# Performance work log

Measured on AMD Instinct MI355X. Metric: run time of the kernel, lower is better.

## Reference

```python
import jax, jax.numpy as jnp
import numpy as np

B, H, W = 8, 256, 256
NF = 64          # num_feat
E = 12           # num_expert
D = NF * 4       # token dim = 256
CD = D * E       # expanded dim = 3072


def _lrelu(x):
    return jnp.where(x >= 0, x, 0.2 * x)


def _conv(x, w, stride, pad):
    return jax.lax.conv_general_dilated(
        x, w, (stride, stride), [(pad, pad), (pad, pad)],
        dimension_numbers=('NCHW', 'OIHW', 'NCHW'))


def _bn(x, g, b):
    # training-mode BatchNorm2d: batch statistics over (N, H, W)
    m = jnp.mean(x, axis=(0, 2, 3), keepdims=True)
    v = jnp.var(x, axis=(0, 2, 3), keepdims=True)
    xn = (x - m) * jax.lax.rsqrt(v + 1e-5)
    return xn * g[None, :, None, None] + b[None, :, None, None]


def setup_inputs() -> dict:
    key = jax.random.key(0)
    ks = jax.random.split(key, 16)
    s = 0.05
    d = {}
    d['x'] = jax.random.normal(ks[0], (B, 3, H, W), jnp.float32)
    d['conv0_w'] = jax.random.normal(ks[1], (NF, 3, 3, 3)) * s
    d['conv0_b'] = jnp.zeros((NF,))
    d['conv1_w'] = jax.random.normal(ks[2], (NF, NF, 4, 4)) * s
    d['bn1_g'] = jnp.ones((NF,)); d['bn1_b'] = jnp.zeros((NF,))
    d['conv2_w'] = jax.random.normal(ks[3], (2 * NF, NF, 3, 3)) * s
    d['bn2_g'] = jnp.ones((2 * NF,)); d['bn2_b'] = jnp.zeros((2 * NF,))
    d['conv3_w'] = jax.random.normal(ks[4], (2 * NF, 2 * NF, 4, 4)) * s
    d['bn3_g'] = jnp.ones((2 * NF,)); d['bn3_b'] = jnp.zeros((2 * NF,))
    d['conv4_w'] = jax.random.normal(ks[5], (4 * NF, 2 * NF, 3, 3)) * s
    d['bn4_g'] = jnp.ones((4 * NF,)); d['bn4_b'] = jnp.zeros((4 * NF,))
    d['conv5_w'] = jax.random.normal(ks[6], (4 * NF, 4 * NF, 3, 3)) * s
    d['bn5_g'] = jnp.ones((4 * NF,)); d['bn5_b'] = jnp.zeros((4 * NF,))
    d['conv6_w'] = jax.random.normal(ks[7], (4 * NF, 4 * NF, 3, 3)) * s
    d['bn6_g'] = jnp.ones((4 * NF,)); d['bn6_b'] = jnp.zeros((4 * NF,))
    d['w_gating'] = jax.random.normal(ks[8], (D, E))          # torch.randn init
    d['body_w'] = jax.random.normal(ks[9], (D, CD)) * s       # Linear(c_dim, c_dim*blocks)
    d['body_b'] = jnp.zeros((CD,))
    d['ortho_w'] = jax.random.normal(ks[10], (1, 1, CD))      # OrthorTransform weight
    d['cls_w1'] = jax.random.normal(ks[11], (D, NF // 2)) * s # shared classifier
    d['cls_b1'] = jnp.zeros((NF // 2,))
    d['cls_w2'] = jax.random.normal(ks[12], (NF // 2, 1)) * s
    d['cls_b2'] = jnp.zeros((1,))
    return d


def reference(x, conv0_w, conv0_b, conv1_w, bn1_g, bn1_b, conv2_w, bn2_g, bn2_b,
              conv3_w, bn3_g, bn3_b, conv4_w, bn4_g, bn4_b, conv5_w, bn5_g, bn5_b,
              conv6_w, bn6_g, bn6_b, w_gating, body_w, body_b, ortho_w,
              cls_w1, cls_b1, cls_w2, cls_b2):
    # --- FE conv stack ---
    h = _lrelu(_conv(x, conv0_w, 1, 1) + conv0_b[None, :, None, None])
    h = _lrelu(_bn(_conv(h, conv1_w, 2, 1), bn1_g, bn1_b))
    h = _lrelu(_bn(_conv(h, conv2_w, 1, 1), bn2_g, bn2_b))
    h = _lrelu(_bn(_conv(h, conv3_w, 2, 1), bn3_g, bn3_b))
    h = _lrelu(_bn(_conv(h, conv4_w, 1, 1), bn4_g, bn4_b))
    h = _lrelu(_bn(_conv(h, conv5_w, 1, 1), bn5_g, bn5_b))
    h = _lrelu(_bn(_conv(h, conv6_w, 1, 1), bn6_g, bn6_b))
    b, c, hh, ww = h.shape
    tok = h.reshape(b, c, hh * ww).transpose(0, 2, 1)            # (B, N, D)
    # --- softmax router ---
    routing = jax.nn.softmax(jnp.einsum('bnd,de->bne', tok, w_gating), axis=-1)
    # --- CodeReduction: Linear + lrelu, OrthorTransform multiply, lrelu ---
    feat = _lrelu(tok @ body_w + body_b)                         # (B, N, E*D)
    feat = _lrelu(feat * ortho_w)
    feat = feat.reshape(b, hh * ww, E, D)                        # torch.split chunks
    # --- shared expert MLP on every chunk (all classifiers alias one module) ---
    hid = _lrelu(jnp.einsum('bned,df->bnef', feat, cls_w1) + cls_b1)
    outs = (jnp.einsum('bnef,fo->bneo', hid, cls_w2) + cls_b2)[..., 0]  # (B,N,E)
    # --- top-1 select (equivalent to the torch.where cascade) ---
    idx = jnp.argmax(routing, axis=-1, keepdims=True)
    output = jnp.take_along_axis(outs, idx, axis=-1)             # (B, N, 1)
    return output
```

## Files before the change

### kernel.cpp

```cpp
#include <hip/hip_runtime.h>

__device__ __forceinline__ float lrelu(float x) { return x >= 0.f ? x : 0.2f * x; }

typedef const __attribute__((address_space(1))) void* gas_ptr;
typedef __attribute__((address_space(3))) void* las_ptr;

__global__ __launch_bounds__(256) void conv0_k(const float* __restrict__ x,
                                               const float* __restrict__ w,
                                               const float* __restrict__ bias,
                                               float* __restrict__ out) {
    __shared__ float sIn[3][34][34];
    __shared__ float sW[27][16];
    const int H = 256;
    int tid = threadIdx.x, tx = tid & 31, ty = tid >> 5;
    int tX = (blockIdx.x & 7) * 32, tY = (blockIdx.x >> 3) * 32;
    int b = blockIdx.y, cog = blockIdx.z * 16;
    float acc[4][16] = {};
    const float* inB = x + (size_t)b * 3 * H * H;
    for (int idx = tid; idx < 3 * 1156; idx += 256) {
        int ci = idx / 1156, r = idx % 1156, iy = r / 34, ix = r % 34;
        int gy = tY - 1 + iy, gx = tX - 1 + ix;
        float v = 0.f;
        if ((unsigned)gy < 256u && (unsigned)gx < 256u)
            v = inB[(ci * H + gy) * H + gx];
// ... 3 lines not shown
        int co = idx & 15, rest = idx >> 4;
        sW[rest][co] = w[(cog + co) * 27 + rest];
    }
    __syncthreads();
#pragma unroll
    for (int ci = 0; ci < 3; ci++)
#pragma unroll
        for (int dy = 0; dy < 3; dy++)
#pragma unroll
            for (int dx = 0; dx < 3; dx++) {
                float a0 = sIn[ci][ty + dy][tx + dx];
                float a1 = sIn[ci][ty + 8 + dy][tx + dx];
                float a2 = sIn[ci][ty + 16 + dy][tx + dx];
                float a3 = sIn[ci][ty + 24 + dy][tx + dx];
                const float* wp = sW[ci * 9 + dy * 3 + dx];
#pragma unroll
                for (int co = 0; co < 16; co++) {
                    float wv = wp[co];
                    acc[0][co] += a0 * wv; acc[1][co] += a1 * wv;
                    acc[2][co] += a2 * wv; acc[3][co] += a3 * wv;
                }
            }
    float* outB = out + (size_t)(b * 64 + cog) * 67080;
#pragma unroll
    for (int co = 0; co < 16; co++) {
        float bv = bias[cog + co];
#pragma unroll
        for (int r = 0; r < 4; r++)
            outB[(size_t)co * 67080 + (size_t)(tY + ty + 8 * r + 1) * 260 +
                 tX + tx + 1] = lrelu(acc[r][co] + bv);
    }
}

template <int COG>
__device__ __forceinline__ void stats_epilogue(float (&acc)[4][COG], float* red,
                                               double2* part, int cog,
                                               int slotBase, int S, int tid) {
#pragma unroll
    for (int c = 0; c < COG; c++) {
        float s = 0.f, q = 0.f;
#pragma unroll
        for (int j = 0; j < 4; j++) { float v = acc[j][c]; s += v; q += v * v; }
        red[c * 256 + tid] = s;
        red[COG * 256 + c * 256 + tid] = q;
    }
    __syncthreads();
    for (int off = 128; off; off >>= 1) {
        if (tid < off) {
#pragma unroll
            for (int c = 0; c < COG; c++) {
                red[c * 256 + tid] += red[c * 256 + tid + off];
                red[COG * 256 + c * 256 + tid] +=
                    red[COG * 256 + c * 256 + tid + off];
            }
        }
        __syncthreads();
    }
    if (tid < COG) {
        int slot = slotBase + blockIdx.y * gridDim.x + blockIdx.x;
        part[(size_t)(cog + tid) * S + slot].x = (double)red[tid * 256];
        part[(size_t)(cog + tid) * S + slot].y =
            (double)red[COG * 256 + tid * 256];
    }
}

template <int COG>
__global__ __launch_bounds__(256) void c4x4p_k(const float* __restrict__ in,
                                               const float* __restrict__ w,
                                               float* __restrict__ out,
                                               double2* __restrict__ part,
                                               int slotBase, int S,
                                               int Cin, int Cout, int Hin,
                                               int Hp, int Wp,
                                               int oHp, int oWp, int oOff) {
    __shared__ float sIn[2][4488];
    __shared__ float sW[2][16 * COG];
    const int Hout = Hin >> 1;
    const int tid = threadIdx.x, tx = tid & 31, ty = tid >> 5;
    const int tpr = Hout >> 5;
    const int tX = (blockIdx.x % tpr) * 32, tY = (blockIdx.x / tpr) * 32;
    const int b = blockIdx.y, cog = blockIdx.z * COG;
    const int HWin = Hp * Wp;
    const float* inB = in + (size_t)b * Cin * HWin;
    const int wvbase = tid & ~63;

    int gOff[5]; int lOff[5]; bool act[5];
#pragma unroll
    for (int r = 0; r < 5; r++) {
        int idx = tid + r * 256;
        bool a = idx < 1122;
        int row = idx / 17, c4 = idx % 17;
        gOff[r] = a ? ((2 * tY + row) * Wp + 2 * tX + 4 * c4) : 0;
        lOff[r] = (r * 256 + wvbase) * 4;
        act[r] = a;
    }
    const int wco = tid % COG, wt = tid / COG;
    const int wgo = ((cog + wco) * Cin) * 16 + wt;
    const bool wact = tid < 16 * COG;

    float acc[4][COG];
#pragma unroll
    for (int j = 0; j < 4; j++)
#pragma unroll
        for (int c = 0; c < COG; c++) acc[j][c] = 0.f;

#pragma unroll
    for (int r = 0; r < 5; r++)
        if (act[r])
            __builtin_amdgcn_global_load_lds((gas_ptr)(inB + gOff[r]),
                                             (las_ptr)(&sIn[0][lOff[r]]), 16, 0, 0);
    if (wact)
        __builtin_amdgcn_global_load_lds((gas_ptr)(w + wgo),
                                         (las_ptr)(&sW[0][wvbase]), 4, 0, 0);
    __syncthreads();

    for (int k = 0; k < Cin; k++) {
        const int cur = k & 1, nb = cur ^ 1;
        const bool more = (k + 1) < Cin;
        if (more) {
            const float* p = inB + (size_t)(k + 1) * HWin;
#pragma unroll
            for (int r = 0; r < 5; r++)
                if (act[r])
                    __builtin_amdgcn_global_load_lds(
                        (gas_ptr)(p + gOff[r]),
                        (las_ptr)(&sIn[nb][lOff[r]]), 16, 0, 0);
            if (wact)
                __builtin_amdgcn_global_load_lds(
                    (gas_ptr)(w + wgo + (k + 1) * 16),
                    (las_ptr)(&sW[nb][wvbase]), 4, 0, 0);
        }
        const float* sI = sIn[cur];
        const float* sw = sW[cur];
#pragma unroll
        for (int dy = 0; dy < 4; dy++)
#pragma unroll
            for (int dx = 0; dx < 4; dx++) {
                const float* bp = sI + (2 * ty + dy) * 68 + 2 * tx + dx;
                float a0 = bp[0];
                float a1 = bp[16 * 68];
                float a2 = bp[32 * 68];
                float a3 = bp[48 * 68];
                const float* wp = sw + (dy * 4 + dx) * COG;
#pragma unroll
                for (int c = 0; c < COG; c++) {
                    float wv = wp[c];
                    acc[0][c] += a0 * wv; acc[1][c] += a1 * wv;
                    acc[2][c] += a2 * wv; acc[3][c] += a3 * wv;
                }
            }
        __syncthreads();
    }

    float* outB = out + (size_t)(b * Cout + cog) * oHp * oWp;
#pragma unroll
    for (int c = 0; c < COG; c++)
#pragma unroll
        for (int r = 0; r < 4; r++)
            outB[(size_t)c * oHp * oWp +
                 (size_t)(tY + ty + 8 * r + oOff) * oWp + tX + tx + oOff] =
                acc[r][c];
    stats_epilogue<COG>(acc, &sIn[0][0], part, cog, slotBase, S, tid);
}

template <int COG>
__global__ __launch_bounds__(256) void c3x3_k(const float* __restrict__ in,
                                              const float* __restrict__ w,
                                              float* __restrict__ out,
                                              double2* __restrict__ part,
                                              int slotBase, int S,
                                              int Cin, int Cout, int H,
                                              int Hp, int Wp,
                                              int oHp, int oWp, int oOff) {
    constexpr int RS = 36;
    constexpr int CI = 34 * RS;
    __shared__ float sIn[2][2 * CI];
    __shared__ float sW[2][18 * COG];
    const int tid = threadIdx.x, tx = tid & 31, ty = tid >> 5;
    const int tpr = H >> 5;
    const int tX = (blockIdx.x % tpr) * 32, tY = (blockIdx.x / tpr) * 32;
    const int b = blockIdx.y, cog = blockIdx.z * COG;
    const int HWin = Hp * Wp;
    const float* inB = in + (size_t)b * Cin * HWin;
    const int wvbase = tid & ~63;

    int gOff[3]; int lOff[3]; bool act[3];
#pragma unroll
    for (int r = 0; r < 3; r++) {
        int idx = tid + r * 256;
        bool a = idx < 612;
        int ci = idx / 306, rem = idx % 306;
        int row = rem / 9, c4 = rem % 9;
        gOff[r] = a ? (ci * HWin + (tY + row) * Wp + tX + 4 * c4) : 0;
        lOff[r] = (r * 256 + wvbase) * 4;
        act[r] = a;
    }
    constexpr int NW = (18 * COG + 255) / 256;
    int wgo[NW]; bool wact[NW];
#pragma unroll
    for (int r = 0; r < NW; r++) {
        int widx = tid + r * 256;
        bool a = widx < 18 * COG;
        int co = widx % COG, rest = widx / COG;
        int ci = rest / 9, t = rest % 9;
        wgo[r] = a ? (((cog + co) * Cin + ci) * 9 + t) : 0;
        wact[r] = a;
    }

    float acc[4][COG];
#pragma unroll
    for (int j = 0; j < 4; j++)
#pragma unroll
        for (int c = 0; c < COG; c++) acc[j][c] = 0.f;

    const int steps = Cin >> 1;

#pragma unroll
    for (int r = 0; r < 3; r++)
        if (act[r])
            __builtin_amdgcn_global_load_lds(
                (gas_ptr)(inB + gOff[r]),
                (las_ptr)(&sIn[0][lOff[r]]), 16, 0, 0);
#pragma unroll
    for (int r = 0; r < NW; r++)
        if (wact[r])
            __builtin_amdgcn_global_load_lds(
                (gas_ptr)(w + wgo[r]),
                (las_ptr)(&sW[0][r * 256 + wvbase]), 4, 0, 0);
    __syncthreads();

    for (int k = 0; k < steps; k++) {
        const int cur = k & 1;
        const int nb = cur ^ 1;
        const bool more = (k + 1) < steps;
        if (more) {
            const int c0n = 2 * (k + 1);
            const float* p = inB + (size_t)c0n * HWin;
            const float* wp2 = w + (size_t)c0n * 9;
#pragma unroll
            for (int r = 0; r < 3; r++)
                if (act[r])
                    __builtin_amdgcn_global_load_lds(
                        (gas_ptr)(p + gOff[r]),
                        (las_ptr)(&sIn[nb][lOff[r]]), 16, 0, 0);
#pragma unroll
            for (int r = 0; r < NW; r++)
                if (wact[r])
                    __builtin_amdgcn_global_load_lds(
                        (gas_ptr)(wp2 + wgo[r]),
                        (las_ptr)(&sW[nb][r * 256 + wvbase]), 4, 0, 0);
        }
        const float* sI = sIn[cur];
        const float* sw = sW[cur];
#pragma unroll
        for (int ci = 0; ci < 2; ci++)
#pragma unroll
            for (int dx = 0; dx < 3; dx++) {
                const float* bp = sI + ci * CI + (4 * ty) * RS + tx + dx;
                float a[6];
#pragma unroll
                for (int j = 0; j < 6; j++) a[j] = bp[j * RS];
#pragma unroll
                for (int dy = 0; dy < 3; dy++) {
                    const float* wp = sw + (ci * 9 + dy * 3 + dx) * COG;
#pragma unroll
                    for (int c = 0; c < COG; c++) {
                        float wv = wp[c];
                        acc[0][c] += a[0 + dy] * wv;
                        acc[1][c] += a[1 + dy] * wv;
                        acc[2][c] += a[2 + dy] * wv;
                        acc[3][c] += a[3 + dy] * wv;
                    }
                }
            }
        __syncthreads();
    }

    float* outB = out + (size_t)(b * Cout + cog) * oHp * oWp;
#pragma unroll
    for (int c = 0; c < COG; c++)
#pragma unroll
        for (int j = 0; j < 4; j++)
            outB[(size_t)c * oHp * oWp +
                 (size_t)(tY + 4 * ty + j + oOff) * oWp + tX + tx + oOff] =
                acc[j][c];
    stats_epilogue<COG>(acc, &sIn[0][0], part, cog, slotBase, S, tid);
}

__global__ void bnfin_k(const double2* __restrict__ part, int S, int C, double invN,
                        const float* __restrict__ g, const float* __restrict__ bb,
                        float2* __restrict__ ss) {
    int c = threadIdx.x;
    if (c >= C) return;
    double sum = 0.0, sq = 0.0;
    for (int s = 0; s < S; s++) {
        double2 p = part[(size_t)c * S + s];
        sum += p.x; sq += p.y;
    }
    double m = sum * invN;
    double v = sq * invN - m * m;
    double sc = (double)g[c] / sqrt(v + 1e-5);
    ss[c] = make_float2((float)sc, (float)((double)bb[c] - m * sc));
}

__global__ __launch_bounds__(256) void bnact_k(float* __restrict__ p,
                                               const float2* __restrict__ ss,
                                               int C, int H, int W,
                                               int Hp, int Wp) {
    int pc = blockIdx.x;
    int c = pc & (C - 1);
    float2 t = ss ? ss[c] : make_float2(1.f, 0.f);
    bool xf = (ss != nullptr);
    float* pl = p + (size_t)pc * Hp * Wp;
    int n = Hp * Wp;
    for (int i = threadIdx.x; i < n; i += 256) {
        int y = i / Wp, x = i - y * Wp;
        bool inter = (y >= 1) && (y <= H) && (x >= 1) && (x <= W);
        if (!inter) pl[i] = 0.f;
        else if (xf) { float v = pl[i]; pl[i] = lrelu(t.x * v + t.y); }
// ... 113 lines not shown
    const float* g5  = (const float*)d_in[16];
    const float* be5 = (const float*)d_in[17];
    const float* w6  = (const float*)d_in[18];
    const float* g6  = (const float*)d_in[19];
    const float* be6 = (const float*)d_in[20];
    const float* wg  = (const float*)d_in[21];
    const float* bw  = (const float*)d_in[22];
    const float* bbp = (const float*)d_in[23];
    const float* owp = (const float*)d_in[24];
    const float* cw1 = (const float*)d_in[25];
    const float* cb1 = (const float*)d_in[26];
    const float* cw2 = (const float*)d_in[27];
    const float* cb2 = (const float*)d_in[28];

    char* W = (char*)d_ws;
    float2* ssb = (float2*)W;
    float2* ss1 = ssb;
    float2* ss2 = ssb + 64;
    float2* ss3 = ssb + 192;
    float2* ss4 = ssb + 320;
    float2* ss5 = ssb + 576;
    float2* ss6 = ssb + 832;
    double2* part = (double2*)(W + 16384);

    char* BIG = W + 278528;
    float* h0p = (float*)(BIG);
    float* h1p = (float*)(BIG + 70287360);
    float* h2p = (float*)(BIG);
    float* h3p = (float*)(BIG + 70287360);
    float* h4p = (float*)(BIG);
    float* h5p = (float*)(BIG + 36765696);
    float* h6  = (float*)(BIG);
    float* tok = (float*)(BIG + 36765696);

    bnact_k<<<256, 256, 0, stream>>>(h0p, nullptr, 64, 256, 256, 258, 260);
    for (int half = 0; half < 2; half++) {
        conv0_k<<<dim3(64, 4, 4), 256, 0, stream>>>(
            x + (size_t)half * 4 * 3 * 65536, w0, b0, h0p);
        c4x4p_k<8><<<dim3(16, 4, 8), 256, 0, stream>>>(
            h0p, w1, h1p + (size_t)half * 4 * 64 * 17160, part, half * 64, 128,
            64, 64, 256, 258, 260, 130, 132, 1);
    }
    bnfin_k<<<1, 256, 0, stream>>>(part, 128, 64, 1.0 / 131072.0, g1, be1, ss1);
    bnact_k<<<512, 256, 0, stream>>>(h1p, ss1, 64, 128, 128, 130, 132);
    c3x3_k<8><<<dim3(16, 8, 16), 256, 0, stream>>>(
        h1p, w2, h2p, part, 0, 128, 64, 128, 128, 130, 132, 130, 132, 1);
    bnfin_k<<<1, 256, 0, stream>>>(part, 128, 128, 1.0 / 131072.0, g2, be2, ss2);
    bnact_k<<<1024, 256, 0, stream>>>(h2p, ss2, 128, 128, 128, 130, 132);
    c4x4p_k<8><<<dim3(4, 8, 16), 256, 0, stream>>>(
        h2p, w3, h3p, part, 0, 32, 128, 128, 128, 130, 132, 66, 68, 1);
    bnfin_k<<<1, 256, 0, stream>>>(part, 32, 128, 1.0 / 32768.0, g3, be3, ss3);
    bnact_k<<<1024, 256, 0, stream>>>(h3p, ss3, 128, 64, 64, 66, 68);
    c3x3_k<8><<<dim3(4, 8, 32), 256, 0, stream>>>(
        h3p, w4, h4p, part, 0, 32, 128, 256, 64, 66, 68, 66, 68, 1);
    bnfin_k<<<1, 256, 0, stream>>>(part, 32, 256, 1.0 / 32768.0, g4, be4, ss4);
    bnact_k<<<2048, 256, 0, stream>>>(h4p, ss4, 256, 64, 64, 66, 68);
    c3x3_k<8><<<dim3(4, 8, 32), 256, 0, stream>>>(
        h4p, w5, h5p, part, 0, 32, 256, 256, 64, 66, 68, 66, 68, 1);
    bnfin_k<<<1, 256, 0, stream>>>(part, 32, 256, 1.0 / 32768.0, g5, be5, ss5);
    bnact_k<<<2048, 256, 0, stream>>>(h5p, ss5, 256, 64, 64, 66, 68);
    c3x3_k<8><<<dim3(4, 8, 32), 256, 0, stream>>>(
        h5p, w6, h6, part, 0, 32, 256, 256, 64, 66, 68, 64, 64, 0);
    bnfin_k<<<1, 256, 0, stream>>>(part, 32, 256, 1.0 / 32768.0, g6, be6, ss6);
    transp_k<<<dim3(128, 8, 8), 256, 0, stream>>>(h6, ss6, tok);
    token_k<<<8192, 256, 0, stream>>>(tok, wg, bw, bbp, owp, cw1, cb1, cw2, cb2,
                                      (float*)d_out);
}
```

Measured before the change: 2.628 ms.

## Parametrize conv tile height and use wave-shuffle BN stats reduction

Adds a rows-per-thread template parameter to the 4x4 stride-2 and 3x3 conv kernels and launches the smaller 64x64 layers and conv1/conv3 with half-height tiles, doubling block counts for better CU occupancy on small grids. The BN partial-stat epilogue now reduces with wave shuffles and a tiny shared buffer instead of a 256-wide shared-memory tree with many barriers. Halving tile height increases halo reloads and weight traffic per output, and doubles partial-stat slots for bnfin.

```diff
diff --git a/kernel.cpp b/kernel.cpp
--- a/kernel.cpp
+++ b/kernel.cpp
@@ -59,39 +59,43 @@
     }
 }
 
-template <int COG>
-__device__ __forceinline__ void stats_epilogue(float (&acc)[4][COG], float* red,
-                                               double2* part, int cog,
-                                               int slotBase, int S, int tid) {
+template <int COG, int RPT>
+__device__ __forceinline__ void stats_epi(float (&acc)[RPT][COG], float2* sRed,
+                                          double2* part, int cog, int slotBase,
+                                          int S, int tid) {
+    const int lane = tid & 63, wv = tid >> 6;
+    float s[COG], q[COG];
 #pragma unroll
     for (int c = 0; c < COG; c++) {
-        float s = 0.f, q = 0.f;
-#pragma unroll
-        for (int j = 0; j < 4; j++) { float v = acc[j][c]; s += v; q += v * v; }
-        red[c * 256 + tid] = s;
-        red[COG * 256 + c * 256 + tid] = q;
-    }
+        float ss = 0.f, qq = 0.f;
+#pragma unroll
+        for (int j = 0; j < RPT; j++) { float v = acc[j][c]; ss += v; qq += v * v; }
+        s[c] = ss; q[c] = qq;
+    }
+#pragma unroll
+    for (int off = 32; off; off >>= 1)
+#pragma unroll
+        for (int c = 0; c < COG; c++) {
+            s[c] += __shfl_xor(s[c], off);
+            q[c] += __shfl_xor(q[c], off);
+        }
+    if (lane == 0)
+#pragma unroll
+        for (int c = 0; c < COG; c++) sRed[wv * COG + c] = make_float2(s[c], q[c]);
     __syncthreads();
-    for (int off = 128; off; off >>= 1) {
-        if (tid < off) {
-#pragma unroll
-            for (int c = 0; c < COG; c++) {
-                red[c * 256 + tid] += red[c * 256 + tid + off];
-                red[COG * 256 + c * 256 + tid] +=
-                    red[COG * 256 + c * 256 + tid + off];
-            }
+    if (tid < COG) {
+        double ss = 0.0, qq = 0.0;
+#pragma unroll
+        for (int wvi = 0; wvi < 4; wvi++) {
+            float2 p = sRed[wvi * COG + tid];
+            ss += (double)p.x; qq += (double)p.y;
         }
-        __syncthreads();
-    }
-    if (tid < COG) {
         int slot = slotBase + blockIdx.y * gridDim.x + blockIdx.x;
-        part[(size_t)(cog + tid) * S + slot].x = (double)red[tid * 256];
-        part[(size_t)(cog + tid) * S + slot].y =
-            (double)red[COG * 256 + tid * 256];
-    }
-}
-
-template <int COG>
+        part[(size_t)(cog + tid) * S + slot] = make_double2(ss, qq);
+    }
+}
+
+template <int COG, int RPT>
 __global__ __launch_bounds__(256) void c4x4p_k(const float* __restrict__ in,
                                                const float* __restrict__ w,
                                                float* __restrict__ out,
@@ -100,22 +104,27 @@
                                                int Cin, int Cout, int Hin,
                                                int Hp, int Wp,
                                                int oHp, int oWp, int oOff) {
-    __shared__ float sIn[2][4488];
+    constexpr int THo = 8 * RPT;
+    constexpr int ROWS = 16 * RPT + 2;
+    constexpr int NSF4 = ROWS * 17;
+    constexpr int NR = (NSF4 + 255) / 256;
+    __shared__ float sIn[2][ROWS * 68];
     __shared__ float sW[2][16 * COG];
+    __shared__ float2 sRed[4 * COG];
     const int Hout = Hin >> 1;
     const int tid = threadIdx.x, tx = tid & 31, ty = tid >> 5;
-    const int tpr = Hout >> 5;
-    const int tX = (blockIdx.x % tpr) * 32, tY = (blockIdx.x / tpr) * 32;
+    const int tpw = Hout >> 5;
+    const int tX = (blockIdx.x % tpw) * 32, tY = (blockIdx.x / tpw) * THo;
     const int b = blockIdx.y, cog = blockIdx.z * COG;
     const int HWin = Hp * Wp;
     const float* inB = in + (size_t)b * Cin * HWin;
     const int wvbase = tid & ~63;
 
-    int gOff[5]; int lOff[5]; bool act[5];
-#pragma unroll
-    for (int r = 0; r < 5; r++) {
+    int gOff[NR]; int lOff[NR]; bool act[NR];
+#pragma unroll
+    for (int r = 0; r < NR; r++) {
         int idx = tid + r * 256;
-        bool a = idx < 1122;
+        bool a = idx < NSF4;
         int row = idx / 17, c4 = idx % 17;
         gOff[r] = a ? ((2 * tY + row) * Wp + 2 * tX + 4 * c4) : 0;
         lOff[r] = (r * 256 + wvbase) * 4;
@@ -125,14 +134,14 @@
     const int wgo = ((cog + wco) * Cin) * 16 + wt;
     const bool wact = tid < 16 * COG;
 
-    float acc[4][COG];
-#pragma unroll
-    for (int j = 0; j < 4; j++)
+    float acc[RPT][COG];
+#pragma unroll
+    for (int j = 0; j < RPT; j++)
 #pragma unroll
         for (int c = 0; c < COG; c++) acc[j][c] = 0.f;
 
 #pragma unroll
-    for (int r = 0; r < 5; r++)
+    for (int r = 0; r < NR; r++)
         if (act[r])
             __builtin_amdgcn_global_load_lds((gas_ptr)(inB + gOff[r]),
                                              (las_ptr)(&sIn[0][lOff[r]]), 16, 0, 0);
@@ -147,7 +156,7 @@
         if (more) {
             const float* p = inB + (size_t)(k + 1) * HWin;
 #pragma unroll
-            for (int r = 0; r < 5; r++)
+            for (int r = 0; r < NR; r++)
                 if (act[r])
                     __builtin_amdgcn_global_load_lds(
                         (gas_ptr)(p + gOff[r]),
@@ -164,16 +173,15 @@
 #pragma unroll
             for (int dx = 0; dx < 4; dx++) {
                 const float* bp = sI + (2 * ty + dy) * 68 + 2 * tx + dx;
-                float a0 = bp[0];
-                float a1 = bp[16 * 68];
-                float a2 = bp[32 * 68];
-                float a3 = bp[48 * 68];
+                float a[RPT];
+#pragma unroll
+                for (int j = 0; j < RPT; j++) a[j] = bp[j * 16 * 68];
                 const float* wp = sw + (dy * 4 + dx) * COG;
 #pragma unroll
                 for (int c = 0; c < COG; c++) {
                     float wv = wp[c];
-                    acc[0][c] += a0 * wv; acc[1][c] += a1 * wv;
-                    acc[2][c] += a2 * wv; acc[3][c] += a3 * wv;
+#pragma unroll
+                    for (int j = 0; j < RPT; j++) acc[j][c] += a[j] * wv;
                 }
             }
         __syncthreads();
@@ -183,14 +191,14 @@
 #pragma unroll
     for (int c = 0; c < COG; c++)
 #pragma unroll
-        for (int r = 0; r < 4; r++)
+        for (int j = 0; j < RPT; j++)
             outB[(size_t)c * oHp * oWp +
-                 (size_t)(tY + ty + 8 * r + oOff) * oWp + tX + tx + oOff] =
-                acc[r][c];
-    stats_epilogue<COG>(acc, &sIn[0][0], part, cog, slotBase, S, tid);
-}
-
-template <int COG>
+                 (size_t)(tY + ty + 8 * j + oOff) * oWp + tX + tx + oOff] =
+                acc[j][c];
+    stats_epi<COG, RPT>(acc, sRed, part, cog, slotBase, S, tid);
+}
+
+template <int COG, int RPT>
 __global__ __launch_bounds__(256) void c3x3_k(const float* __restrict__ in,
                                               const float* __restrict__ w,
                                               float* __restrict__ out,
@@ -199,24 +207,29 @@
                                               int Cin, int Cout, int H,
                                               int Hp, int Wp,
                                               int oHp, int oWp, int oOff) {
+    constexpr int TH = 8 * RPT;
     constexpr int RS = 36;
-    constexpr int CI = 34 * RS;
+    constexpr int ROWS = TH + 2;
+    constexpr int CI = ROWS * RS;
+    constexpr int NSF4 = 2 * ROWS * 9;
+    constexpr int NR = (NSF4 + 255) / 256;
     __shared__ float sIn[2][2 * CI];
     __shared__ float sW[2][18 * COG];
+    __shared__ float2 sRed[4 * COG];
     const int tid = threadIdx.x, tx = tid & 31, ty = tid >> 5;
-    const int tpr = H >> 5;
-    const int tX = (blockIdx.x % tpr) * 32, tY = (blockIdx.x / tpr) * 32;
+    const int tpw = H >> 5;
+    const int tX = (blockIdx.x % tpw) * 32, tY = (blockIdx.x / tpw) * TH;
     const int b = blockIdx.y, cog = blockIdx.z * COG;
     const int HWin = Hp * Wp;
     const float* inB = in + (size_t)b * Cin * HWin;
     const int wvbase = tid & ~63;
 
-    int gOff[3]; int lOff[3]; bool act[3];
-#pragma unroll
-    for (int r = 0; r < 3; r++) {
+    int gOff[NR]; int lOff[NR]; bool act[NR];
+#pragma unroll
+    for (int r = 0; r < NR; r++) {
         int idx = tid + r * 256;
-        bool a = idx < 612;
-        int ci = idx / 306, rem = idx % 306;
+        bool a = idx < NSF4;
+        int ci = idx / (9 * ROWS), rem = idx % (9 * ROWS);
         int row = rem / 9, c4 = rem % 9;
         gOff[r] = a ? (ci * HWin + (tY + row) * Wp + tX + 4 * c4) : 0;
         lOff[r] = (r * 256 + wvbase) * 4;
@@ -234,16 +247,16 @@
         wact[r] = a;
     }
 
-    float acc[4][COG];
-#pragma unroll
-    for (int j = 0; j < 4; j++)
+    float acc[RPT][COG];
+#pragma unroll
+    for (int j = 0; j < RPT; j++)
 #pragma unroll
         for (int c = 0; c < COG; c++) acc[j][c] = 0.f;
 
     const int steps = Cin >> 1;
 
 #pragma unroll
-    for (int r = 0; r < 3; r++)
+    for (int r = 0; r < NR; r++)
         if (act[r])
             __builtin_amdgcn_global_load_lds(
                 (gas_ptr)(inB + gOff[r]),
@@ -265,7 +278,7 @@
             const float* p = inB + (size_t)c0n * HWin;
             const float* wp2 = w + (size_t)c0n * 9;
 #pragma unroll
-            for (int r = 0; r < 3; r++)
+            for (int r = 0; r < NR; r++)
                 if (act[r])
                     __builtin_amdgcn_global_load_lds(
                         (gas_ptr)(p + gOff[r]),
@@ -283,20 +296,19 @@
         for (int ci = 0; ci < 2; ci++)
 #pragma unroll
             for (int dx = 0; dx < 3; dx++) {
-                const float* bp = sI + ci * CI + (4 * ty) * RS + tx + dx;
-                float a[6];
-#pragma unroll
-                for (int j = 0; j < 6; j++) a[j] = bp[j * RS];
+                const float* bp = sI + ci * CI + (RPT * ty) * RS + tx + dx;
+                float a[RPT + 2];
+#pragma unroll
+                for (int j = 0; j < RPT + 2; j++) a[j] = bp[j * RS];
 #pragma unroll
                 for (int dy = 0; dy < 3; dy++) {
                     const float* wp = sw + (ci * 9 + dy * 3 + dx) * COG;
 #pragma unroll
                     for (int c = 0; c < COG; c++) {
                         float wv = wp[c];
-                        acc[0][c] += a[0 + dy] * wv;
-                        acc[1][c] += a[1 + dy] * wv;
-                        acc[2][c] += a[2 + dy] * wv;
-                        acc[3][c] += a[3 + dy] * wv;
+#pragma unroll
+                        for (int j = 0; j < RPT; j++)
+                            acc[j][c] += a[j + dy] * wv;
                     }
                 }
             }
@@ -307,11 +319,11 @@
 #pragma unroll
     for (int c = 0; c < COG; c++)
 #pragma unroll
-        for (int j = 0; j < 4; j++)
+        for (int j = 0; j < RPT; j++)
             outB[(size_t)c * oHp * oWp +
-                 (size_t)(tY + 4 * ty + j + oOff) * oWp + tX + tx + oOff] =
+                 (size_t)(tY + RPT * ty + j + oOff) * oWp + tX + tx + oOff] =
                 acc[j][c];
-    stats_epilogue<COG>(acc, &sIn[0][0], part, cog, slotBase, S, tid);
+    stats_epi<COG, RPT>(acc, sRed, part, cog, slotBase, S, tid);
 }
 
 __global__ void bnfin_k(const double2* __restrict__ part, int S, int C, double invN,
@@ -496,31 +508,31 @@
     for (int half = 0; half < 2; half++) {
         conv0_k<<<dim3(64, 4, 4), 256, 0, stream>>>(
             x + (size_t)half * 4 * 3 * 65536, w0, b0, h0p);
-        c4x4p_k<8><<<dim3(16, 4, 8), 256, 0, stream>>>(
-            h0p, w1, h1p + (size_t)half * 4 * 64 * 17160, part, half * 64, 128,
+        c4x4p_k<8, 2><<<dim3(32, 4, 8), 256, 0, stream>>>(
+            h0p, w1, h1p + (size_t)half * 4 * 64 * 17160, part, half * 128, 256,
             64, 64, 256, 258, 260, 130, 132, 1);
     }
-    bnfin_k<<<1, 256, 0, stream>>>(part, 128, 64, 1.0 / 131072.0, g1, be1, ss1);
+    bnfin_k<<<1, 256, 0, stream>>>(part, 256, 64, 1.0 / 131072.0, g1, be1, ss1);
     bnact_k<<<512, 256, 0, stream>>>(h1p, ss1, 64, 128, 128, 130, 132);
-    c3x3_k<8><<<dim3(16, 8, 16), 256, 0, stream>>>(
+    c3x3_k<8, 4><<<dim3(16, 8, 16), 256, 0, stream>>>(
         h1p, w2, h2p, part, 0, 128, 64, 128, 128, 130, 132, 130, 132, 1);
     bnfin_k<<<1, 256, 0, stream>>>(part, 128, 128, 1.0 / 131072.0, g2, be2, ss2);
     bnact_k<<<1024, 256, 0, stream>>>(h2p, ss2, 128, 128, 128, 130, 132);
-    c4x4p_k<8><<<dim3(4, 8, 16), 256, 0, stream>>>(
-        h2p, w3, h3p, part, 0, 32, 128, 128, 128, 130, 132, 66, 68, 1);
-    bnfin_k<<<1, 256, 0, stream>>>(part, 32, 128, 1.0 / 32768.0, g3, be3, ss3);
+    c4x4p_k<8, 2><<<dim3(8, 8, 16), 256, 0, stream>>>(
+        h2p, w3, h3p, part, 0, 64, 128, 128, 128, 130, 132, 66, 68, 1);
+    bnfin_k<<<1, 256, 0, stream>>>(part, 64, 128, 1.0 / 32768.0, g3, be3, ss3);
     bnact_k<<<1024, 256, 0, stream>>>(h3p, ss3, 128, 64, 64, 66, 68);
-    c3x3_k<8><<<dim3(4, 8, 32), 256, 0, stream>>>(
-        h3p, w4, h4p, part, 0, 32, 128, 256, 64, 66, 68, 66, 68, 1);
-    bnfin_k<<<1, 256, 0, stream>>>(part, 32, 256, 1.0 / 32768.0, g4, be4, ss4);
+    c3x3_k<8, 2><<<dim3(8, 8, 32), 256, 0, stream>>>(
+        h3p, w4, h4p, part, 0, 64, 128, 256, 64, 66, 68, 66, 68, 1);
+    bnfin_k<<<1, 256, 0, stream>>>(part, 64, 256, 1.0 / 32768.0, g4, be4, ss4);
     bnact_k<<<2048, 256, 0, stream>>>(h4p, ss4, 256, 64, 64, 66, 68);
-    c3x3_k<8><<<dim3(4, 8, 32), 256, 0, stream>>>(
-        h4p, w5, h5p, part, 0, 32, 256, 256, 64, 66, 68, 66, 68, 1);
-    bnfin_k<<<1, 256, 0, stream>>>(part, 32, 256, 1.0 / 32768.0, g5, be5, ss5);
+    c3x3_k<8, 2><<<dim3(8, 8, 32), 256, 0, stream>>>(
+        h4p, w5, h5p, part, 0, 64, 256, 256, 64, 66, 68, 66, 68, 1);
+    bnfin_k<<<1, 256, 0, stream>>>(part, 64, 256, 1.0 / 32768.0, g5, be5, ss5);
     bnact_k<<<2048, 256, 0, stream>>>(h5p, ss5, 256, 64, 64, 66, 68);
-    c3x3_k<8><<<dim3(4, 8, 32), 256, 0, stream>>>(
-        h5p, w6, h6, part, 0, 32, 256, 256, 64, 66, 68, 64, 64, 0);
-    bnfin_k<<<1, 256, 0, stream>>>(part, 32, 256, 1.0 / 32768.0, g6, be6, ss6);
+    c3x3_k<8, 2><<<dim3(8, 8, 32), 256, 0, stream>>>(
+        h5p, w6, h6, part, 0, 64, 256, 256, 64, 66, 68, 64, 64, 0);
+    bnfin_k<<<1, 256, 0, stream>>>(part, 64, 256, 1.0 / 32768.0, g6, be6, ss6);
     transp_k<<<dim3(128, 8, 8), 256, 0, stream>>>(h6, ss6, tok);
     token_k<<<8192, 256, 0, stream>>>(tok, wg, bw, bbp, owp, cw1, cb1, cw2, cb2,
                                       (float*)d_out);
```

Result: slower. 2.756 ms (+4.9%).

## Triple-buffer conv input staging with explicit vmcnt waits and wave-shuffle BN stats

Applied to the files above, without the earlier changes.

The 4x4 stride-2 and 3x3 conv kernels now use a three-stage LDS ring with async global-to-LDS loads issued two steps ahead. Each step waits on a fixed vmcnt count followed by a single s_barrier, replacing the double buffer with a full __syncthreads per step. To keep the per-wave vmcnt counts uniform, waves that would otherwise issue no load for a slot issue a dummy load into a scratch LDS buffer. The BN statistics epilogue is replaced by wave shuffles plus a small cross-wave reduction, removing a long tree of shared-memory stages and barriers. In exchange the kernels use more LDS per block, which may lower occupancy, and the hand-written vmcnt values are fragile.

```diff
diff --git a/kernel.cpp b/kernel.cpp
--- a/kernel.cpp
+++ b/kernel.cpp
@@ -60,34 +60,38 @@
 }
 
 template <int COG>
-__device__ __forceinline__ void stats_epilogue(float (&acc)[4][COG], float* red,
-                                               double2* part, int cog,
-                                               int slotBase, int S, int tid) {
+__device__ __forceinline__ void stats_epi(float (&acc)[4][COG], float2* sRed,
+                                          double2* part, int cog, int slotBase,
+                                          int S, int tid) {
+    const int lane = tid & 63, wv = tid >> 6;
+    float s[COG], q[COG];
 #pragma unroll
     for (int c = 0; c < COG; c++) {
-        float s = 0.f, q = 0.f;
-#pragma unroll
-        for (int j = 0; j < 4; j++) { float v = acc[j][c]; s += v; q += v * v; }
-        red[c * 256 + tid] = s;
-        red[COG * 256 + c * 256 + tid] = q;
-    }
+        float ss = 0.f, qq = 0.f;
+#pragma unroll
+        for (int j = 0; j < 4; j++) { float v = acc[j][c]; ss += v; qq += v * v; }
+        s[c] = ss; q[c] = qq;
+    }
+#pragma unroll
+    for (int off = 32; off; off >>= 1)
+#pragma unroll
+        for (int c = 0; c < COG; c++) {
+            s[c] += __shfl_xor(s[c], off);
+            q[c] += __shfl_xor(q[c], off);
+        }
+    if (lane == 0)
+#pragma unroll
+        for (int c = 0; c < COG; c++) sRed[wv * COG + c] = make_float2(s[c], q[c]);
     __syncthreads();
-    for (int off = 128; off; off >>= 1) {
-        if (tid < off) {
-#pragma unroll
-            for (int c = 0; c < COG; c++) {
-                red[c * 256 + tid] += red[c * 256 + tid + off];
-                red[COG * 256 + c * 256 + tid] +=
-                    red[COG * 256 + c * 256 + tid + off];
-            }
+    if (tid < COG) {
+        double ss = 0.0, qq = 0.0;
+#pragma unroll
+        for (int wvi = 0; wvi < 4; wvi++) {
+            float2 p = sRed[wvi * COG + tid];
+            ss += (double)p.x; qq += (double)p.y;
         }
-        __syncthreads();
-    }
-    if (tid < COG) {
         int slot = slotBase + blockIdx.y * gridDim.x + blockIdx.x;
-        part[(size_t)(cog + tid) * S + slot].x = (double)red[tid * 256];
-        part[(size_t)(cog + tid) * S + slot].y =
-            (double)red[COG * 256 + tid * 256];
+        part[(size_t)(cog + tid) * S + slot] = make_double2(ss, qq);
     }
 }
 
@@ -100,10 +104,14 @@
                                                int Cin, int Cout, int Hin,
                                                int Hp, int Wp,
                                                int oHp, int oWp, int oOff) {
-    __shared__ float sIn[2][4488];
-    __shared__ float sW[2][16 * COG];
+    constexpr int NSF4 = 1122;
+    __shared__ float sIn[3][4488];
+    __shared__ float sW[3][16 * COG];
+    __shared__ float2 sRed[4 * COG];
+    __shared__ alignas(16) float sDummy[64];
     const int Hout = Hin >> 1;
     const int tid = threadIdx.x, tx = tid & 31, ty = tid >> 5;
+    const bool lane0 = (tid & 63) == 0;
     const int tpr = Hout >> 5;
     const int tX = (blockIdx.x % tpr) * 32, tY = (blockIdx.x / tpr) * 32;
     const int b = blockIdx.y, cog = blockIdx.z * COG;
@@ -111,19 +119,20 @@
     const float* inB = in + (size_t)b * Cin * HWin;
     const int wvbase = tid & ~63;
 
-    int gOff[5]; int lOff[5]; bool act[5];
+    int gOff[5]; int lOff[5]; bool act[5]; bool aw[5];
 #pragma unroll
     for (int r = 0; r < 5; r++) {
         int idx = tid + r * 256;
-        bool a = idx < 1122;
+        act[r] = idx < NSF4;
+        aw[r] = (r * 256 + wvbase) < NSF4;
         int row = idx / 17, c4 = idx % 17;
-        gOff[r] = a ? ((2 * tY + row) * Wp + 2 * tX + 4 * c4) : 0;
+        gOff[r] = act[r] ? ((2 * tY + row) * Wp + 2 * tX + 4 * c4) : 0;
         lOff[r] = (r * 256 + wvbase) * 4;
-        act[r] = a;
     }
     const int wco = tid % COG, wt = tid / COG;
     const int wgo = ((cog + wco) * Cin) * 16 + wt;
     const bool wact = tid < 16 * COG;
+    const bool waw = wvbase < 16 * COG;
 
     float acc[4][COG];
 #pragma unroll
@@ -131,32 +140,36 @@
 #pragma unroll
         for (int c = 0; c < COG; c++) acc[j][c] = 0.f;
 
-#pragma unroll
-    for (int r = 0; r < 5; r++)
-        if (act[r])
-            __builtin_amdgcn_global_load_lds((gas_ptr)(inB + gOff[r]),
-                                             (las_ptr)(&sIn[0][lOff[r]]), 16, 0, 0);
-    if (wact)
-        __builtin_amdgcn_global_load_lds((gas_ptr)(w + wgo),
-                                         (las_ptr)(&sW[0][wvbase]), 4, 0, 0);
-    __syncthreads();
-
-    for (int k = 0; k < Cin; k++) {
-        const int cur = k & 1, nb = cur ^ 1;
-        const bool more = (k + 1) < Cin;
-        if (more) {
-            const float* p = inB + (size_t)(k + 1) * HWin;
-#pragma unroll
-            for (int r = 0; r < 5; r++)
-                if (act[r])
-                    __builtin_amdgcn_global_load_lds(
-                        (gas_ptr)(p + gOff[r]),
-                        (las_ptr)(&sIn[nb][lOff[r]]), 16, 0, 0);
-            if (wact)
-                __builtin_amdgcn_global_load_lds(
-                    (gas_ptr)(w + wgo + (k + 1) * 16),
-                    (las_ptr)(&sW[nb][wvbase]), 4, 0, 0);
+    auto STAGE = [&](int t, int buf) {
+        const float* p = inB + (size_t)t * HWin;
+#pragma unroll
+        for (int r = 0; r < 5; r++) {
+            float* dst = act[r] ? &sIn[buf][lOff[r]] : sDummy;
+            const float* src = act[r] ? (p + gOff[r]) : p;
+            if (act[r] || (!aw[r] && lane0))
+                __builtin_amdgcn_global_load_lds((gas_ptr)src, (las_ptr)dst,
+                                                 16, 0, 0);
         }
+        {
+            const float* wsrc = wact ? (w + wgo + t * 16) : w;
+            float* wdst = wact ? &sW[buf][wvbase] : sDummy;
+            if (wact || (!waw && lane0))
+                __builtin_amdgcn_global_load_lds((gas_ptr)wsrc, (las_ptr)wdst,
+                                                 4, 0, 0);
+        }
+    };
+
+    const int steps = Cin;
+    STAGE(0, 0);
+    STAGE(1, 1);
+    int cur = 0, nx2 = 2;
+    for (int k = 0; k < steps; k++) {
+        if (k < steps - 1) asm volatile("s_waitcnt vmcnt(6)" ::: "memory");
+        else               asm volatile("s_waitcnt vmcnt(0)" ::: "memory");
+        __builtin_amdgcn_sched_barrier(0);
+        __builtin_amdgcn_s_barrier();
+        __builtin_amdgcn_sched_barrier(0);
+        if (k + 2 < steps) STAGE(k + 2, nx2);
         const float* sI = sIn[cur];
         const float* sw = sW[cur];
 #pragma unroll
@@ -176,7 +189,8 @@
                     acc[2][c] += a2 * wv; acc[3][c] += a3 * wv;
                 }
             }
-        __syncthreads();
+        cur = (cur == 2) ? 0 : cur + 1;
+        nx2 = (nx2 == 2) ? 0 : nx2 + 1;
     }
 
     float* outB = out + (size_t)(b * Cout + cog) * oHp * oWp;
@@ -187,7 +201,7 @@
             outB[(size_t)c * oHp * oWp +
                  (size_t)(tY + ty + 8 * r + oOff) * oWp + tX + tx + oOff] =
                 acc[r][c];
-    stats_epilogue<COG>(acc, &sIn[0][0], part, cog, slotBase, S, tid);
+    stats_epi<COG>(acc, sRed, part, cog, slotBase, S, tid);
 }
 
 template <int COG>
@@ -201,9 +215,13 @@
                                               int oHp, int oWp, int oOff) {
     constexpr int RS = 36;
     constexpr int CI = 34 * RS;
-    __shared__ float sIn[2][2 * CI];
-    __shared__ float sW[2][18 * COG];
+    constexpr int NSF4 = 612;
+    __shared__ float sIn[3][2 * CI];
+    __shared__ float sW[3][18 * COG];
+    __shared__ float2 sRed[4 * COG];
+    __shared__ alignas(16) float sDummy[64];
     const int tid = threadIdx.x, tx = tid & 31, ty = tid >> 5;
+    const bool lane0 = (tid & 63) == 0;
     const int tpr = H >> 5;
     const int tX = (blockIdx.x % tpr) * 32, tY = (blockIdx.x / tpr) * 32;
     const int b = blockIdx.y, cog = blockIdx.z * COG;
@@ -211,27 +229,24 @@
     const float* inB = in + (size_t)b * Cin * HWin;
     const int wvbase = tid & ~63;
 
-    int gOff[3]; int lOff[3]; bool act[3];
+    int gOff[3]; int lOff[3]; bool act[3]; bool aw[3];
 #pragma unroll
     for (int r = 0; r < 3; r++) {
         int idx = tid + r * 256;
-        bool a = idx < 612;
+        act[r] = idx < NSF4;
+        aw[r] = (r * 256 + wvbase) < NSF4;
         int ci = idx / 306, rem = idx % 306;
         int row = rem / 9, c4 = rem % 9;
-        gOff[r] = a ? (ci * HWin + (tY + row) * Wp + tX + 4 * c4) : 0;
+        gOff[r] = act[r] ? (ci * HWin + (tY + row) * Wp + tX + 4 * c4) : 0;
         lOff[r] = (r * 256 + wvbase) * 4;
-        act[r] = a;
-    }
-    constexpr int NW = (18 * COG + 255) / 256;
-    int wgo[NW]; bool wact[NW];
-#pragma unroll
-    for (int r = 0; r < NW; r++) {
-        int widx = tid + r * 256;
-        bool a = widx < 18 * COG;
-        int co = widx % COG, rest = widx / COG;
+    }
+    const bool wact = tid < 18 * COG;
+    const bool waw = wvbase < 18 * COG;
+    int wgo;
+    {
+        int co = tid % COG, rest = tid / COG;
         int ci = rest / 9, t = rest % 9;
-        wgo[r] = a ? (((cog + co) * Cin + ci) * 9 + t) : 0;
-        wact[r] = a;
+        wgo = ((cog + co) * Cin + ci) * 9 + t;
     }
 
     float acc[4][COG];
@@ -240,43 +255,36 @@
 #pragma unroll
         for (int c = 0; c < COG; c++) acc[j][c] = 0.f;
 
+    auto STAGE = [&](int t, int buf) {
+        const float* p = inB + (size_t)(2 * t) * HWin;
+#pragma unroll
+        for (int r = 0; r < 3; r++) {
+            float* dst = act[r] ? &sIn[buf][lOff[r]] : sDummy;
+            const float* src = act[r] ? (p + gOff[r]) : p;
+            if (act[r] || (!aw[r] && lane0))
+                __builtin_amdgcn_global_load_lds((gas_ptr)src, (las_ptr)dst,
+                                                 16, 0, 0);
+        }
+        {
+            const float* wsrc = wact ? (w + (size_t)(2 * t) * 9 + wgo) : w;
+            float* wdst = wact ? &sW[buf][wvbase] : sDummy;
+            if (wact || (!waw && lane0))
+                __builtin_amdgcn_global_load_lds((gas_ptr)wsrc, (las_ptr)wdst,
+                                                 4, 0, 0);
+        }
+    };
+
     const int steps = Cin >> 1;
-
-#pragma unroll
-    for (int r = 0; r < 3; r++)
-        if (act[r])
-            __builtin_amdgcn_global_load_lds(
-                (gas_ptr)(inB + gOff[r]),
-                (las_ptr)(&sIn[0][lOff[r]]), 16, 0, 0);
-#pragma unroll
-    for (int r = 0; r < NW; r++)
-        if (wact[r])
-            __builtin_amdgcn_global_load_lds(
-                (gas_ptr)(w + wgo[r]),
-                (las_ptr)(&sW[0][r * 256 + wvbase]), 4, 0, 0);
-    __syncthreads();
-
+    STAGE(0, 0);
+    STAGE(1, 1);
+    int cur = 0, nx2 = 2;
     for (int k = 0; k < steps; k++) {
-        const int cur = k & 1;
-        const int nb = cur ^ 1;
-        const bool more = (k + 1) < steps;
-        if (more) {
-            const int c0n = 2 * (k + 1);
-            const float* p = inB + (size_t)c0n * HWin;
-            const float* wp2 = w + (size_t)c0n * 9;
-#pragma unroll
-            for (int r = 0; r < 3; r++)
-                if (act[r])
-                    __builtin_amdgcn_global_load_lds(
-                        (gas_ptr)(p + gOff[r]),
-                        (las_ptr)(&sIn[nb][lOff[r]]), 16, 0, 0);
-#pragma unroll
-            for (int r = 0; r < NW; r++)
-                if (wact[r])
-                    __builtin_amdgcn_global_load_lds(
-                        (gas_ptr)(wp2 + wgo[r]),
-                        (las_ptr)(&sW[nb][r * 256 + wvbase]), 4, 0, 0);
-        }
+        if (k < steps - 1) asm volatile("s_waitcnt vmcnt(4)" ::: "memory");
+        else               asm volatile("s_waitcnt vmcnt(0)" ::: "memory");
+        __builtin_amdgcn_sched_barrier(0);
+        __builtin_amdgcn_s_barrier();
+        __builtin_amdgcn_sched_barrier(0);
+        if (k + 2 < steps) STAGE(k + 2, nx2);
         const float* sI = sIn[cur];
         const float* sw = sW[cur];
 #pragma unroll
@@ -300,7 +308,8 @@
                     }
                 }
             }
-        __syncthreads();
+        cur = (cur == 2) ? 0 : cur + 1;
+        nx2 = (nx2 == 2) ? 0 : nx2 + 1;
     }
 
     float* outB = out + (size_t)(b * Cout + cog) * oHp * oWp;
@@ -311,7 +320,7 @@
             outB[(size_t)c * oHp * oWp +
                  (size_t)(tY + 4 * ty + j + oOff) * oWp + tX + tx + oOff] =
                 acc[j][c];
-    stats_epilogue<COG>(acc, &sIn[0][0], part, cog, slotBase, S, tid);
+    stats_epi<COG>(acc, sRed, part, cog, slotBase, S, tid);
 }
 
 __global__ void bnfin_k(const double2* __restrict__ part, int S, int C, double invN,
```

Result: no change. 2.668 ms (+1.5%).

## Pre-transpose conv weights and read them directly instead of staging in LDS

Applied to the files above, without the earlier changes.

Adds a weight transpose kernel that reorders each conv weight into (ci, tap, co) layout, so the conv kernels read weights straight from global memory with uniform, contiguous per-output-channel loads. This drops the LDS weight staging and its async copies. The block-level BN statistic reduction moves from a shared-memory tree with many barriers to wavefront shuffles plus a small cross-wave sum. The cost is extra transpose launches and scratch space, and weight reads now depend on scalar/cache loads inside the inner loop.

```diff
diff --git a/kernel.cpp b/kernel.cpp
--- a/kernel.cpp
+++ b/kernel.cpp
@@ -59,41 +59,56 @@
     }
 }
 
+__global__ __launch_bounds__(256) void wtr_k(const float* __restrict__ in,
+                                             float* __restrict__ out,
+                                             int Cout, int Cin, int T) {
+    int i = blockIdx.x * 256 + threadIdx.x;
+    int n = Cout * Cin * T;
+    if (i >= n) return;
+    int co = i % Cout; int rest = i / Cout;
+    int t = rest % T;  int ci = rest / T;
+    out[i] = in[(co * Cin + ci) * T + t];
+}
+
 template <int COG>
-__device__ __forceinline__ void stats_epilogue(float (&acc)[4][COG], float* red,
-                                               double2* part, int cog,
-                                               int slotBase, int S, int tid) {
+__device__ __forceinline__ void stats_epi(float (&acc)[4][COG], float2* sRed,
+                                          double2* part, int cog, int slotBase,
+                                          int S, int tid) {
+    const int lane = tid & 63, wv = tid >> 6;
+    float s[COG], q[COG];
 #pragma unroll
     for (int c = 0; c < COG; c++) {
-        float s = 0.f, q = 0.f;
-#pragma unroll
-        for (int j = 0; j < 4; j++) { float v = acc[j][c]; s += v; q += v * v; }
-        red[c * 256 + tid] = s;
-        red[COG * 256 + c * 256 + tid] = q;
-    }
+        float ss = 0.f, qq = 0.f;
+#pragma unroll
+        for (int j = 0; j < 4; j++) { float v = acc[j][c]; ss += v; qq += v * v; }
+        s[c] = ss; q[c] = qq;
+    }
+#pragma unroll
+    for (int off = 32; off; off >>= 1)
+#pragma unroll
+        for (int c = 0; c < COG; c++) {
+            s[c] += __shfl_xor(s[c], off);
+            q[c] += __shfl_xor(q[c], off);
+        }
+    if (lane == 0)
+#pragma unroll
+        for (int c = 0; c < COG; c++) sRed[wv * COG + c] = make_float2(s[c], q[c]);
     __syncthreads();
-    for (int off = 128; off; off >>= 1) {
-        if (tid < off) {
-#pragma unroll
-            for (int c = 0; c < COG; c++) {
-                red[c * 256 + tid] += red[c * 256 + tid + off];
-                red[COG * 256 + c * 256 + tid] +=
-                    red[COG * 256 + c * 256 + tid + off];
-            }
+    if (tid < COG) {
+        double ss = 0.0, qq = 0.0;
+#pragma unroll
+        for (int wvi = 0; wvi < 4; wvi++) {
+            float2 p = sRed[wvi * COG + tid];
+            ss += (double)p.x; qq += (double)p.y;
         }
-        __syncthreads();
-    }
-    if (tid < COG) {
         int slot = slotBase + blockIdx.y * gridDim.x + blockIdx.x;
-        part[(size_t)(cog + tid) * S + slot].x = (double)red[tid * 256];
-        part[(size_t)(cog + tid) * S + slot].y =
-            (double)red[COG * 256 + tid * 256];
+        part[(size_t)(cog + tid) * S + slot] = make_double2(ss, qq);
     }
 }
 
 template <int COG>
 __global__ __launch_bounds__(256) void c4x4p_k(const float* __restrict__ in,
-                                               const float* __restrict__ w,
+                                               const float* __restrict__ wT,
                                                float* __restrict__ out,
                                                double2* __restrict__ part,
                                                int slotBase, int S,
@@ -101,7 +116,7 @@
                                                int Hp, int Wp,
                                                int oHp, int oWp, int oOff) {
     __shared__ float sIn[2][4488];
-    __shared__ float sW[2][16 * COG];
+    __shared__ float2 sRed[4 * COG];
     const int Hout = Hin >> 1;
     const int tid = threadIdx.x, tx = tid & 31, ty = tid >> 5;
     const int tpr = Hout >> 5;
@@ -121,9 +136,6 @@
         lOff[r] = (r * 256 + wvbase) * 4;
         act[r] = a;
     }
-    const int wco = tid % COG, wt = tid / COG;
-    const int wgo = ((cog + wco) * Cin) * 16 + wt;
-    const bool wact = tid < 16 * COG;
 
     float acc[4][COG];
 #pragma unroll
@@ -136,9 +148,6 @@
         if (act[r])
             __builtin_amdgcn_global_load_lds((gas_ptr)(inB + gOff[r]),
                                              (las_ptr)(&sIn[0][lOff[r]]), 16, 0, 0);
-    if (wact)
-        __builtin_amdgcn_global_load_lds((gas_ptr)(w + wgo),
-                                         (las_ptr)(&sW[0][wvbase]), 4, 0, 0);
     __syncthreads();
 
     for (int k = 0; k < Cin; k++) {
@@ -152,13 +161,9 @@
                     __builtin_amdgcn_global_load_lds(
                         (gas_ptr)(p + gOff[r]),
                         (las_ptr)(&sIn[nb][lOff[r]]), 16, 0, 0);
-            if (wact)
-                __builtin_amdgcn_global_load_lds(
-                    (gas_ptr)(w + wgo + (k + 1) * 16),
-                    (las_ptr)(&sW[nb][wvbase]), 4, 0, 0);
         }
         const float* sI = sIn[cur];
-        const float* sw = sW[cur];
+        const float* wb = wT + (size_t)k * 16 * Cout + cog;
 #pragma unroll
         for (int dy = 0; dy < 4; dy++)
 #pragma unroll
@@ -168,7 +173,7 @@
                 float a1 = bp[16 * 68];
                 float a2 = bp[32 * 68];
                 float a3 = bp[48 * 68];
-                const float* wp = sw + (dy * 4 + dx) * COG;
+                const float* wp = wb + (dy * 4 + dx) * Cout;
 #pragma unroll
                 for (int c = 0; c < COG; c++) {
                     float wv = wp[c];
@@ -187,12 +192,12 @@
             outB[(size_t)c * oHp * oWp +
                  (size_t)(tY + ty + 8 * r + oOff) * oWp + tX + tx + oOff] =
                 acc[r][c];
-    stats_epilogue<COG>(acc, &sIn[0][0], part, cog, slotBase, S, tid);
+    stats_epi<COG>(acc, sRed, part, cog, slotBase, S, tid);
 }
 
 template <int COG>
 __global__ __launch_bounds__(256) void c3x3_k(const float* __restrict__ in,
-                                              const float* __restrict__ w,
+                                              const float* __restrict__ wT,
                                               float* __restrict__ out,
                                               double2* __restrict__ part,
                                               int slotBase, int S,
@@ -202,7 +207,7 @@
     constexpr int RS = 36;
     constexpr int CI = 34 * RS;
     __shared__ float sIn[2][2 * CI];
-    __shared__ float sW[2][18 * COG];
+    __shared__ float2 sRed[4 * COG];
     const int tid = threadIdx.x, tx = tid & 31, ty = tid >> 5;
     const int tpr = H >> 5;
     const int tX = (blockIdx.x % tpr) * 32, tY = (blockIdx.x / tpr) * 32;
@@ -222,17 +227,6 @@
         lOff[r] = (r * 256 + wvbase) * 4;
         act[r] = a;
     }
-    constexpr int NW = (18 * COG + 255) / 256;
-    int wgo[NW]; bool wact[NW];
-#pragma unroll
-    for (int r = 0; r < NW; r++) {
-        int widx = tid + r * 256;
-        bool a = widx < 18 * COG;
-        int co = widx % COG, rest = widx / COG;
-        int ci = rest / 9, t = rest % 9;
-        wgo[r] = a ? (((cog + co) * Cin + ci) * 9 + t) : 0;
-        wact[r] = a;
-    }
 
     float acc[4][COG];
 #pragma unroll
@@ -248,12 +242,6 @@
             __builtin_amdgcn_global_load_lds(
                 (gas_ptr)(inB + gOff[r]),
                 (las_ptr)(&sIn[0][lOff[r]]), 16, 0, 0);
-#pragma unroll
-    for (int r = 0; r < NW; r++)
-        if (wact[r])
-            __builtin_amdgcn_global_load_lds(
-                (gas_ptr)(w + wgo[r]),
-                (las_ptr)(&sW[0][r * 256 + wvbase]), 4, 0, 0);
     __syncthreads();
 
     for (int k = 0; k < steps; k++) {
@@ -263,24 +251,17 @@
         if (more) {
             const int c0n = 2 * (k + 1);
             const float* p = inB + (size_t)c0n * HWin;
-            const float* wp2 = w + (size_t)c0n * 9;
 #pragma unroll
             for (int r = 0; r < 3; r++)
                 if (act[r])
                     __builtin_amdgcn_global_load_lds(
                         (gas_ptr)(p + gOff[r]),
                         (las_ptr)(&sIn[nb][lOff[r]]), 16, 0, 0);
-#pragma unroll
-            for (int r = 0; r < NW; r++)
-                if (wact[r])
-                    __builtin_amdgcn_global_load_lds(
-                        (gas_ptr)(wp2 + wgo[r]),
-                        (las_ptr)(&sW[nb][r * 256 + wvbase]), 4, 0, 0);
         }
         const float* sI = sIn[cur];
-        const float* sw = sW[cur];
-#pragma unroll
-        for (int ci = 0; ci < 2; ci++)
+#pragma unroll
+        for (int ci = 0; ci < 2; ci++) {
+            const float* wbc = wT + ((size_t)(2 * k + ci) * 9) * Cout + cog;
 #pragma unroll
             for (int dx = 0; dx < 3; dx++) {
                 const float* bp = sI + ci * CI + (4 * ty) * RS + tx + dx;
@@ -289,7 +270,7 @@
                 for (int j = 0; j < 6; j++) a[j] = bp[j * RS];
 #pragma unroll
                 for (int dy = 0; dy < 3; dy++) {
-                    const float* wp = sw + (ci * 9 + dy * 3 + dx) * COG;
+                    const float* wp = wbc + (dy * 3 + dx) * Cout;
 #pragma unroll
                     for (int c = 0; c < COG; c++) {
                         float wv = wp[c];
@@ -300,6 +281,7 @@
                     }
                 }
             }
+        }
         __syncthreads();
     }
 
@@ -311,7 +293,7 @@
             outB[(size_t)c * oHp * oWp +
                  (size_t)(tY + 4 * ty + j + oOff) * oWp + tX + tx + oOff] =
                 acc[j][c];
-    stats_epilogue<COG>(acc, &sIn[0][0], part, cog, slotBase, S, tid);
+    stats_epi<COG>(acc, sRed, part, cog, slotBase, S, tid);
 }
 
 __global__ void bnfin_k(const double2* __restrict__ part, int S, int C, double invN,
@@ -491,35 +473,47 @@
     float* h5p = (float*)(BIG + 36765696);
     float* h6  = (float*)(BIG);
     float* tok = (float*)(BIG + 36765696);
-
+    float* wT1 = (float*)(BIG + 105431040);
+    float* wT2 = (float*)(BIG + 105693184);
+    float* wT3 = (float*)(BIG + 105988096);
+    float* wT4 = (float*)(BIG + 88670208);
+    float* wT5 = (float*)(BIG + 89849856);
+    float* wT6 = (float*)(BIG + 92209152);
+
+    wtr_k<<<256, 256, 0, stream>>>(w1, wT1, 64, 64, 16);
+    wtr_k<<<288, 256, 0, stream>>>(w2, wT2, 128, 64, 9);
+    wtr_k<<<1024, 256, 0, stream>>>(w3, wT3, 128, 128, 16);
     bnact_k<<<256, 256, 0, stream>>>(h0p, nullptr, 64, 256, 256, 258, 260);
     for (int half = 0; half < 2; half++) {
         conv0_k<<<dim3(64, 4, 4), 256, 0, stream>>>(
             x + (size_t)half * 4 * 3 * 65536, w0, b0, h0p);
         c4x4p_k<8><<<dim3(16, 4, 8), 256, 0, stream>>>(
-            h0p, w1, h1p + (size_t)half * 4 * 64 * 17160, part, half * 64, 128,
+            h0p, wT1, h1p + (size_t)half * 4 * 64 * 17160, part, half * 64, 128,
             64, 64, 256, 258, 260, 130, 132, 1);
     }
     bnfin_k<<<1, 256, 0, stream>>>(part, 128, 64, 1.0 / 131072.0, g1, be1, ss1);
     bnact_k<<<512, 256, 0, stream>>>(h1p, ss1, 64, 128, 128, 130, 132);
     c3x3_k<8><<<dim3(16, 8, 16), 256, 0, stream>>>(
-        h1p, w2, h2p, part, 0, 128, 64, 128, 128, 130, 132, 130, 132, 1);
+        h1p, wT2, h2p, part, 0, 128, 64, 128, 128, 130, 132, 130, 132, 1);
     bnfin_k<<<1, 256, 0, stream>>>(part, 128, 128, 1.0 / 131072.0, g2, be2, ss2);
     bnact_k<<<1024, 256, 0, stream>>>(h2p, ss2, 128, 128, 128, 130, 132);
     c4x4p_k<8><<<dim3(4, 8, 16), 256, 0, stream>>>(
-        h2p, w3, h3p, part, 0, 32, 128, 128, 128, 130, 132, 66, 68, 1);
+        h2p, wT3, h3p, part, 0, 32, 128, 128, 128, 130, 132, 66, 68, 1);
+    wtr_k<<<1152, 256, 0, stream>>>(w4, wT4, 256, 128, 9);
+    wtr_k<<<2304, 256, 0, stream>>>(w5, wT5, 256, 256, 9);
+    wtr_k<<<2304, 256, 0, stream>>>(w6, wT6, 256, 256, 9);
     bnfin_k<<<1, 256, 0, stream>>>(part, 32, 128, 1.0 / 32768.0, g3, be3, ss3);
     bnact_k<<<1024, 256, 0, stream>>>(h3p, ss3, 128, 64, 64, 66, 68);
     c3x3_k<8><<<dim3(4, 8, 32), 256, 0, stream>>>(
-        h3p, w4, h4p, part, 0, 32, 128, 256, 64, 66, 68, 66, 68, 1);
+        h3p, wT4, h4p, part, 0, 32, 128, 256, 64, 66, 68, 66, 68, 1);
     bnfin_k<<<1, 256, 0, stream>>>(part, 32, 256, 1.0 / 32768.0, g4, be4, ss4);
     bnact_k<<<2048, 256, 0, stream>>>(h4p, ss4, 256, 64, 64, 66, 68);
     c3x3_k<8><<<dim3(4, 8, 32), 256, 0, stream>>>(
-        h4p, w5, h5p, part, 0, 32, 256, 256, 64, 66, 68, 66, 68, 1);
+        h4p, wT5, h5p, part, 0, 32, 256, 256, 64, 66, 68, 66, 68, 1);
     bnfin_k<<<1, 256, 0, stream>>>(part, 32, 256, 1.0 / 32768.0, g5, be5, ss5);
     bnact_k<<<2048, 256, 0, stream>>>(h5p, ss5, 256, 64, 64, 66, 68);
     c3x3_k<8><<<dim3(4, 8, 32), 256, 0, stream>>>(
-        h5p, w6, h6, part, 0, 32, 256, 256, 64, 66, 68, 64, 64, 0);
+        h5p, wT6, h6, part, 0, 32, 256, 256, 64, 66, 68, 64, 64, 0);
     bnfin_k<<<1, 256, 0, stream>>>(part, 32, 256, 1.0 / 32768.0, g6, be6, ss6);
     transp_k<<<dim3(128, 8, 8), 256, 0, stream>>>(h6, ss6, tok);
     token_k<<<8192, 256, 0, stream>>>(tok, wg, bw, bbp, owp, cw1, cb1, cw2, cb2,
```

New measurement: 2.706 ms. +3.0%, slower.
